# Optimization experiments

Measured on AMD Instinct MI355X. Metric: run time of the kernel, lower is better.

Reference implementation:

```python
import jax, jax.numpy as jnp
import numpy as np
import math

B, S, D = 2, 2048, 1024
H, HD = 16, 64
ROT = 16          # rotary_dim = head_dim * 0.25
FF = 4096
EPS = 1e-5


def setup_inputs() -> dict:
    key = jax.random.key(0)
    ks = jax.random.split(key, 12)
    sc = lambda *sh: 0.02
    inp = {
        "x": jax.random.normal(ks[0], (B, S, D), jnp.float32),
        "attention_mask": jnp.tril(jnp.ones((S, S), bool))[None, None],  # causal [1,1,S,S]
        "W_qkv": jax.random.normal(ks[1], (3 * D, D), jnp.float32) * 0.02,
        "b_qkv": jnp.zeros((3 * D,), jnp.float32),
        "W_o": jax.random.normal(ks[2], (D, D), jnp.float32) * 0.02,
        "b_o": jnp.zeros((D,), jnp.float32),
        "ln1_w": jnp.ones((D,), jnp.float32),
        "ln1_b": jnp.zeros((D,), jnp.float32),
        "ln2_w": jnp.ones((D,), jnp.float32),
        "ln2_b": jnp.zeros((D,), jnp.float32),
        "W1": jax.random.normal(ks[3], (FF, D), jnp.float32) * 0.02,
        "b1": jnp.zeros((FF,), jnp.float32),
        "W2": jax.random.normal(ks[4], (D, FF), jnp.float32) * 0.02,
        "b2": jnp.zeros((D,), jnp.float32),
    }
    # real rotary frequencies, shaped [1,1,S,ROT//2,2]
    inv_freq = 1.0 / (10000.0 ** (jnp.arange(0, ROT, 2, dtype=jnp.float32) / ROT))
    t = jnp.arange(S, dtype=jnp.float32)
    ang = t[:, None] * inv_freq[None, :]                      # [S, ROT//2]
    inp["freqs_cis"] = jnp.stack([jnp.cos(ang), jnp.sin(ang)], -1)[None, None]
    return inp


def layer_norm(x, w, b):
    mu = jnp.mean(x, -1, keepdims=True)
    var = jnp.mean(jnp.square(x - mu), -1, keepdims=True)
    return (x - mu) * jax.lax.rsqrt(var + EPS) * w + b


def apply_rotate_emb(x, freqs_cis):
    # x: [B,H,S,ROT]; freqs_cis: [1,1,S,ROT//2,2]
    x1, x2 = x[..., : ROT // 2], x[..., ROT // 2 :]
    cos, sin = freqs_cis[..., 0], freqs_cis[..., 1]
    return jnp.concatenate([x1 * cos - x2 * sin, x1 * sin + x2 * cos], -1)


def reference(x, attention_mask, freqs_cis, W_qkv, b_qkv, W_o, b_o,
              ln1_w, ln1_b, ln2_w, ln2_b, W1, b1, W2, b2):
    h = layer_norm(x, ln1_w, ln1_b)
    qkv = jnp.einsum("bsd,ed->bse", h, W_qkv) + b_qkv
    q, k, v = jnp.split(qkv, 3, axis=-1)
    to_heads = lambda t: t.reshape(B, S, H, HD).transpose(0, 2, 1, 3)  # [B,H,S,HD]
    q, k, v = to_heads(q), to_heads(k), to_heads(v)
    q = jnp.concatenate([apply_rotate_emb(q[..., :ROT], freqs_cis), q[..., ROT:]], -1)
    k = jnp.concatenate([apply_rotate_emb(k[..., :ROT], freqs_cis), k[..., ROT:]], -1)
    scores = jnp.einsum("bhqd,bhkd->bhqk", q, k) / math.sqrt(HD)
    scores = jnp.where(attention_mask, scores, -jnp.inf)
    probs = jax.nn.softmax(scores, axis=-1)
    out = jnp.einsum("bhqk,bhkd->bhqd", probs, v)
    out = out.transpose(0, 2, 1, 3).reshape(B, S, D)
    attn_out = jnp.einsum("bsd,ed->bse", out, W_o) + b_o
    # parallel residual (dropout is identity in eval)
    h2 = layer_norm(x, ln2_w, ln2_b)
    ff = jnp.einsum("bsf,df->bsd", jax.nn.gelu(jnp.einsum("bsd,fd->bsf", h2, W1) + b1, approximate=False), W2) + b2
    return x + ff + attn_out
```

## Files before the change

kernel.cpp:

```cpp
#include <hip/hip_runtime.h>

#define DEV __device__ __forceinline__

typedef __bf16 bf16;
typedef bf16 bf16x4 __attribute__((ext_vector_type(4)));
typedef bf16 bf16x8 __attribute__((ext_vector_type(8)));
typedef float f32x4 __attribute__((ext_vector_type(4)));

DEV f32x4 mfma16(bf16x8 a, bf16x8 b, f32x4 c) {
  return __builtin_amdgcn_mfma_f32_16x16x32_bf16(a, b, c, 0, 0, 0);
}

DEV void gload_lds16(const bf16* g, bf16* l) {
  __builtin_amdgcn_global_load_lds((const __attribute__((address_space(1))) void*)g,
                                   (__attribute__((address_space(3))) void*)l, 16, 0, 0);
}

#define PH_BAR __builtin_amdgcn_s_barrier()
#define VM(NSTR) asm volatile("s_waitcnt vmcnt(" NSTR ")" ::: "memory")
#define WAITBAR(NSTR) asm volatile("s_waitcnt vmcnt(" NSTR ")\n\ts_barrier" ::: "memory")

DEV float fast_gelu(float x) {
  const float z = x * x;
  const float w = __builtin_fmaf(z, 0.1029353f, 2.3019853f);
  const float e = __builtin_amdgcn_exp2f(x * w);
  const float r = __builtin_amdgcn_rcpf(1.0f + e);
  return x - x * r;
}

__global__ __launch_bounds__(256) void ln_dual(
    const float* __restrict__ x,
    const float* __restrict__ w1, const float* __restrict__ b1,
    const float* __restrict__ w2, const float* __restrict__ b2,
    bf16* __restrict__ h1, bf16* __restrict__ h2)
{
  __shared__ float red[2][4];
  const int row = blockIdx.x, t = threadIdx.x;
  const int lane = t & 63, wave = t >> 6;
  const float4 v = ((const float4*)(x + (size_t)row * 1024))[t];
  float vv[4] = {v.x, v.y, v.z, v.w};
  float s = vv[0] + vv[1] + vv[2] + vv[3];
  float q = vv[0]*vv[0] + vv[1]*vv[1] + vv[2]*vv[2] + vv[3]*vv[3];
  #pragma unroll
  for (int o = 32; o; o >>= 1) { s += __shfl_xor(s, o); q += __shfl_xor(q, o); }
  if (lane == 0) { red[0][wave] = s; red[1][wave] = q; }
  __syncthreads();
  s = red[0][0] + red[0][1] + red[0][2] + red[0][3];
  q = red[1][0] + red[1][1] + red[1][2] + red[1][3];
  const float mu = s * (1.0f / 1024.0f);
  const float var = q * (1.0f / 1024.0f) - mu * mu;
  const float rs = rsqrtf(var + 1e-5f);
  bf16x4 o1, o2;
  #pragma unroll
  for (int j = 0; j < 4; ++j) {
    const int i = t * 4 + j;
    const float xh = (vv[j] - mu) * rs;
    o1[j] = (bf16)(xh * w1[i] + b1[i]);
    o2[j] = (bf16)(xh * w2[i] + b2[i]);
  }
  *(bf16x4*)&h1[(size_t)row * 1024 + t * 4] = o1;
  *(bf16x4*)&h2[(size_t)row * 1024 + t * 4] = o2;
}

__global__ __launch_bounds__(256) void cast_all(
    const float* __restrict__ Wqkv_f, const float* __restrict__ W1_f,
    const float* __restrict__ Wo_f, const float* __restrict__ W2_f,
    bf16* __restrict__ wQKV, bf16* __restrict__ w1, bf16* __restrict__ wCat)
{
  const int b = blockIdx.x, t = threadIdx.x;
  if (b < 3072) {
    const int i = b * 256 + t;
    const float4 v = ((const float4*)Wqkv_f)[i];
    bf16x4 o = {(bf16)v.x, (bf16)v.y, (bf16)v.z, (bf16)v.w};
    ((bf16x4*)wQKV)[i] = o;
  } else if (b < 7168) {
    const int i = (b - 3072) * 256 + t;
    const float4 v = ((const float4*)W1_f)[i];
    bf16x4 o = {(bf16)v.x, (bf16)v.y, (bf16)v.z, (bf16)v.w};
    ((bf16x4*)w1)[i] = o;
  } else if (b < 8192) {
    const int row = b - 7168;
    const float4 v = *(const float4*)&Wo_f[(size_t)row * 1024 + t * 4];
    bf16x4 o = {(bf16)v.x, (bf16)v.y, (bf16)v.z, (bf16)v.w};
    *(bf16x4*)&wCat[(size_t)row * 5120 + t * 4] = o;
  } else {
    const int row = b - 8192;
    #pragma unroll
    for (int k = 0; k < 4; ++k) {
      const int col = t * 4 + k * 1024;
      const float4 v = *(const float4*)&W2_f[(size_t)row * 4096 + col];
      bf16x4 o = {(bf16)v.x, (bf16)v.y, (bf16)v.z, (bf16)v.w};
      *(bf16x4*)&wCat[(size_t)row * 5120 + 1024 + col] = o;
    }
  }
}

DEV bf16x8 ldfrag(const bf16* unit, int lr, int g) {
  return *(const bf16x8*)&unit[lr * 32 + ((g ^ ((lr >> 1) & 3)) << 3)];
}
DEV void read_bfr(const bf16* unit, int blr, int g, bf16x8 bfr[4]) {
  #pragma unroll
  for (int nj = 0; nj < 4; ++nj) bfr[nj] = ldfrag(unit, blr + nj * 16, g);
}
DEV void read_af(const bf16* unit, int alr, int g, bf16x8 af[4]) {
  #pragma unroll
  for (int ml = 0; ml < 4; ++ml) af[ml] = ldfrag(unit, alr + ml * 16, g);
}
DEV void do_mfma(const bf16x8 af[4], const bf16x8 bfr[4], f32x4 acc[8][4], int mh) {
  __builtin_amdgcn_s_setprio(1);
  #pragma unroll
  for (int ml = 0; ml < 4; ++ml)
    #pragma unroll
    for (int nj = 0; nj < 4; ++nj)
      acc[mh * 4 + ml][nj] = mfma16(af[ml], bfr[nj], acc[mh * 4 + ml][nj]);
  __builtin_amdgcn_s_setprio(0);
}

template <int EPI>
__global__ __launch_bounds__(512) void gemm256(
    const bf16* __restrict__ A, const bf16* __restrict__ B,
    const float* __restrict__ bias, void* __restrict__ Cv,
    float* __restrict__ P1, float* __restrict__ P2, float* __restrict__ P3,
    int K, int ldc, int ntiles, int nbx, int nkt)
{
  __shared__ __align__(16) bf16 As[2][2][2][4096];
  __shared__ __align__(16) bf16 Bs[2][2][2][4096];
  const int tid = threadIdx.x;
  const int lane = tid & 63, wave = tid >> 6;
  const int wm = wave >> 2, wn = wave & 3;
  const int g = lane >> 4, c = lane & 15;
  const int cpx = gridDim.x >> 3;
  const int swz = ((int)blockIdx.x & 7) * cpx + ((int)blockIdx.x >> 3);
  const int tile = swz % ntiles;
  const int sk = swz / ntiles;
  const int bm = (tile / nbx) * 256, bn = (tile % nbx) * 256;

  const int slr = tid >> 2;
  const int sch = (tid & 3) ^ ((tid >> 3) & 3);
  const bf16* aU[2][2];
  const bf16* bU[2][2];
  {
    const bf16* a0 = A + (size_t)(bm + ((slr >> 6) * 128) + (slr & 63)) * K
                       + (size_t)sk * nkt * 64 + sch * 8;
    const bf16* b0 = B + (size_t)(bn + slr) * K + (size_t)sk * nkt * 64 + sch * 8;
    aU[0][0] = a0;            aU[0][1] = a0 + (size_t)64 * K;
    aU[1][0] = a0 + 32;       aU[1][1] = a0 + (size_t)64 * K + 32;
    bU[0][0] = b0;            bU[0][1] = b0 + (size_t)128 * K;
    bU[1][0] = b0 + 32;       bU[1][1] = b0 + (size_t)128 * K + 32;
  }
#define STG_A(bf_, kkh_, ub_, ko_) gload_lds16(aU[kkh_][ub_] + (ko_), &As[bf_][kkh_][ub_][wave * 512])
#define STG_B(bf_, kkh_, ub_, ko_) gload_lds16(bU[kkh_][ub_] + (ko_), &Bs[bf_][kkh_][ub_][wave * 512])

  f32x4 acc[8][4] = {};
  bf16x8 bfr[4], af[4];
  const int alr = (wm << 6) + c;
  const int blr = ((wn & 1) << 6) + c;
  const int bub = wn >> 1;

  STG_B(0, 0, 0, 0); STG_B(0, 0, 1, 0); STG_A(0, 0, 0, 0); STG_A(0, 0, 1, 0);
  STG_B(0, 1, 0, 0); STG_B(0, 1, 1, 0); STG_A(0, 1, 0, 0); STG_A(0, 1, 1, 0);
  WAITBAR("4");

  for (int t = 0; t < nkt - 1; ++t) {
    const int buf = t & 1, nxt = buf ^ 1;
    const int ko = (t + 1) * 64;
    read_bfr(&Bs[buf][0][bub][0], blr, g, bfr);
    read_af(&As[buf][0][0][0], alr, g, af);
    STG_B(nxt, 0, 0, ko); STG_B(nxt, 0, 1, ko);
    PH_BAR;
    do_mfma(af, bfr, acc, 0);
    PH_BAR;
    read_af(&As[buf][0][1][0], alr, g, af);
    STG_A(nxt, 0, 0, ko); STG_A(nxt, 0, 1, ko);
    PH_BAR;
    do_mfma(af, bfr, acc, 1);
    VM("4");
    PH_BAR;
    read_bfr(&Bs[buf][1][bub][0], blr, g, bfr);
    read_af(&As[buf][1][0][0], alr, g, af);
    STG_B(nxt, 1, 0, ko); STG_B(nxt, 1, 1, ko);
    PH_BAR;
    do_mfma(af, bfr, acc, 0);
    PH_BAR;
    read_af(&As[buf][1][1][0], alr, g, af);
    STG_A(nxt, 1, 0, ko); STG_A(nxt, 1, 1, ko);
    PH_BAR;
    do_mfma(af, bfr, acc, 1);
    VM("4");
    PH_BAR;
  }
  {
    const int buf = (nkt - 1) & 1;
    read_bfr(&Bs[buf][0][bub][0], blr, g, bfr);
    read_af(&As[buf][0][0][0], alr, g, af);
    PH_BAR;
    do_mfma(af, bfr, acc, 0);
    PH_BAR;
    read_af(&As[buf][0][1][0], alr, g, af);
    PH_BAR;
    do_mfma(af, bfr, acc, 1);
    VM("0");
    PH_BAR;
    read_bfr(&Bs[buf][1][bub][0], blr, g, bfr);
    read_af(&As[buf][1][0][0], alr, g, af);
    PH_BAR;
    do_mfma(af, bfr, acc, 0);
    PH_BAR;
    read_af(&As[buf][1][1][0], alr, g, af);
    PH_BAR;
    do_mfma(af, bfr, acc, 1);
  }
#undef STG_A
#undef STG_B

  float* Pp = nullptr;
  if constexpr (EPI == 2) Pp = (sk == 1) ? P1 : (sk == 2) ? P2 : (sk == 3) ? P3 : (float*)Cv;
  const int row0 = bm + wm * 128 + 4 * g;
  const int col0 = bn + wn * 64 + c;
  #pragma unroll
  for (int mi = 0; mi < 8; ++mi) {
    #pragma unroll
    for (int nj = 0; nj < 4; ++nj) {
      const int col = col0 + nj * 16;
      float bv = 0.0f;
      if constexpr (EPI < 2) bv = bias[col];
      #pragma unroll
      for (int r = 0; r < 4; ++r) {
        const size_t idx = (size_t)(row0 + mi * 16 + r) * ldc + col;
        float vo = acc[mi][nj][r] + bv;
        if constexpr (EPI == 0) {
          ((bf16*)Cv)[idx] = (bf16)vo;
        } else if constexpr (EPI == 1) {
          ((bf16*)Cv)[idx] = (bf16)fast_gelu(vo);
        } else {
          Pp[idx] = vo;
        }
      }
    }
  }
}

__global__ __launch_bounds__(256) void combine_out(
    const float* __restrict__ p0, const float* __restrict__ p1,
    const float* __restrict__ p2, const float* __restrict__ x,
    const float* __restrict__ bo, const float* __restrict__ b2,
    float* __restrict__ out)
{
  const int row = blockIdx.x, t = threadIdx.x;
  const size_t base = (size_t)row * 1024 + t * 4;
  float4 a = *(float4*)&out[base];
  const float4 v0 = *(const float4*)&p0[base];
  const float4 v1 = *(const float4*)&p1[base];
  const float4 v2 = *(const float4*)&p2[base];
  const float4 vx = *(const float4*)&x[base];
  const float4 vb = *(const float4*)&bo[t * 4];
  const float4 vc = *(const float4*)&b2[t * 4];
  a.x += v0.x + v1.x + v2.x + vx.x + vb.x + vc.x;
  a.y += v0.y + v1.y + v2.y + vx.y + vb.y + vc.y;
  a.z += v0.z + v1.z + v2.z + vx.z + vb.z + vc.z;
  a.w += v0.w + v1.w + v2.w + vx.w + vb.w + vc.w;
  *(float4*)&out[base] = a;
}

__global__ __launch_bounds__(256) void rope_reshape(
    const bf16* __restrict__ qkv, const float* __restrict__ freqs,
    bf16* __restrict__ Q, bf16* __restrict__ K, bf16* __restrict__ VT)
{
  __shared__ bf16 vt[64][72];
  const int t = threadIdx.x;
  const int bh = blockIdx.y, b = bh >> 4, h = bh & 15;
  const int sc = blockIdx.x * 64;
  const int sl = t >> 2, s = sc + sl;
  const int d0 = (t & 3) * 16;

  const size_t rowbase = (size_t)(b * 2048 + s) * 3072 + h * 64 + d0;
  const size_t obase = ((size_t)bh * 2048 + s) * 64 + d0;

  #pragma unroll
  for (int which = 0; which < 2; ++which) {
    const bf16* src = qkv + rowbase + which * 1024;
    bf16x8 v0 = *(const bf16x8*)src;
    bf16x8 v1 = *(const bf16x8*)(src + 8);
    if (d0 == 0) {
      bf16x8 r0, r1;
      #pragma unroll
      for (int j = 0; j < 8; ++j) {
        const float cs = freqs[s * 16 + j * 2];
        const float sn = freqs[s * 16 + j * 2 + 1];
        const float x1 = (float)v0[j], x2 = (float)v1[j];
        r0[j] = (bf16)(x1 * cs - x2 * sn);
        r1[j] = (bf16)(x1 * sn + x2 * cs);
      }
      v0 = r0; v1 = r1;
    }
    bf16* dst = (which == 0 ? Q : K) + obase;
    *(bf16x8*)dst = v0;
    *(bf16x8*)(dst + 8) = v1;
  }
  {
    const bf16* src = qkv + rowbase + 2048;
    bf16x8 v0 = *(const bf16x8*)src;
    bf16x8 v1 = *(const bf16x8*)(src + 8);
    #pragma unroll
    for (int j = 0; j < 8; ++j) { vt[sl][d0 + j] = v0[j]; vt[sl][d0 + 8 + j] = v1[j]; }
  }
  __syncthreads();
  {
    const int d = t >> 2;
    const int s0 = (t & 3) * 16;
    bf16x8 o0, o1;
    #pragma unroll
    for (int j = 0; j < 8; ++j) { o0[j] = vt[s0 + j][d]; o1[j] = vt[s0 + 8 + j][d]; }
    bf16* dst = VT + ((size_t)bh * 64 + d) * 2048 + sc + s0;
    *(bf16x8*)dst = o0;
    *(bf16x8*)(dst + 8) = o1;
  }
}

__global__ __launch_bounds__(512, 4) void attn_kernel(
    const bf16* __restrict__ Q, const bf16* __restrict__ Kg,
    const bf16* __restrict__ VTg, bf16* __restrict__ O, int ldO)
{
  __shared__ __align__(16) bf16 Ks[3][64][64];
  __shared__ __align__(16) bf16 Vs[3][64][64];
  __shared__ __align__(16) bf16 Ps[8][16][64];

  const int tid = threadIdx.x;
  const int lane = tid & 63, wave = tid >> 6;
  const int g = lane >> 4, c = lane & 15;
  const int L = blockIdx.x;
  const int half = L >> 8, r = L & 255;
  const int bh = (half << 4) | (r >> 4);
  const int qtile = half ? (15 - (r & 15)) : (r & 15);
  const int qw = qtile * 128 + wave * 16;

  const bf16* Qp = Q + (size_t)bh * 2048 * 64;
  const bf16* Kp = Kg + (size_t)bh * 2048 * 64;
  const bf16* Vp = VTg + (size_t)bh * 64 * 2048;

  const int srow = lane >> 3;
  const int schunk = (lane & 7) ^ srow;
  const int svr = wave * 8 + srow;
  const size_t kdelta = (size_t)64 * 64;

  bf16x8 qreg[2];
  {
    const float qs = 0.125f * 1.44269504f;
    bf16x8 t0 = *(const bf16x8*)&Qp[(size_t)(qw + c) * 64 + g * 8];
    bf16x8 t1 = *(const bf16x8*)&Qp[(size_t)(qw + c) * 64 + 32 + g * 8];
    #pragma unroll
    for (int j = 0; j < 8; ++j) {
      qreg[0][j] = (bf16)((float)t0[j] * qs);
      qreg[1][j] = (bf16)((float)t1[j] * qs);
    }
  }
  bf16x8 ones;
  #pragma unroll
  for (int j = 0; j < 8; ++j) ones[j] = (bf16)1.0f;

  const int cq = c & 7;
  int fo[4][2];
  #pragma unroll
  for (int i = 0; i < 4; ++i)
    #pragma unroll
    for (int kk = 0; kk < 2; ++kk)
      fo[i][kk] = (i * 16 + c) * 64 + (((kk * 4 + g) ^ cq) << 3);
  bf16* pw[4];
  #pragma unroll
  for (int kf = 0; kf < 4; ++kf)
    pw[kf] = &Ps[wave][c][((((kf * 2 + (g >> 1)) ^ cq) << 3)) + ((g & 1) << 2)];
  const bf16* pr[2];
  #pragma unroll
  for (int kk = 0; kk < 2; ++kk)
    pr[kk] = &Ps[wave][c][((kk * 4 + g) ^ cq) << 3];
  const bf16* ks0 = &Ks[0][0][0];
  const bf16* vs0 = &Vs[0][0][0];

  f32x4 oacc[4] = {};
  f32x4 lacc = {};
  float m_ = -1e30f;

  const int nkb = 2 * qtile + 2;
#define STAGE(j_, b3_) do {                                                        \
    gload_lds16(&Kp[(size_t)((j_) * 64 + svr) * 64 + schunk * 8], &Ks[b3_][wave * 8][0]); \
    gload_lds16(&Vp[(size_t)svr * 2048 + (j_) * 64 + schunk * 8], &Vs[b3_][wave * 8][0]); \
  } while (0)

  auto qkt = [&](f32x4* st, int bufi) {
    const bf16* kt = ks0 + bufi * kdelta;
    __builtin_amdgcn_s_setprio(1);
    #pragma unroll
    for (int kf = 0; kf < 4; ++kf) {
      f32x4 z = {};
      z = mfma16(*(const bf16x8*)(kt + fo[kf][0]), qreg[0], z);
      st[kf] = mfma16(*(const bf16x8*)(kt + fo[kf][1]), qreg[1], z);
    }
    __builtin_amdgcn_s_setprio(0);
  };

  auto smpv = [&](const f32x4* st, int j_, int bufi) {
    const int kbase = j_ * 64;
    float v[16];
    if (kbase + 63 > qw) {
      const int qrel = qw + c - kbase;
      #pragma unroll
      for (int kf = 0; kf < 4; ++kf)
        #pragma unroll
        for (int rr = 0; rr < 4; ++rr)
          v[kf * 4 + rr] = (kf * 16 + 4 * g + rr <= qrel) ? st[kf][rr] : -1e30f;
    } else {
      #pragma unroll
      for (int kf = 0; kf < 4; ++kf)
        #pragma unroll
        for (int rr = 0; rr < 4; ++rr)
          v[kf * 4 + rr] = st[kf][rr];
    }
    float u0 = fmaxf(fmaxf(v[0], v[1]), v[2]);
    float u1 = fmaxf(fmaxf(v[3], v[4]), v[5]);
    float u2 = fmaxf(fmaxf(v[6], v[7]), v[8]);
    float u3 = fmaxf(fmaxf(v[9], v[10]), v[11]);
    float u4 = fmaxf(fmaxf(v[12], v[13]), v[14]);
    float tm = fmaxf(fmaxf(fmaxf(u0, u1), u2), fmaxf(fmaxf(u3, u4), v[15]));
    if (__any(tm > m_ + 8.0f)) {
      float tr = fmaxf(tm, __shfl_xor(tm, 16));
      tr = fmaxf(tr, __shfl_xor(tr, 32));
      const float mn = fmaxf(m_, tr);
      const float alpha = __builtin_amdgcn_exp2f(m_ - mn);
      m_ = mn;
      lacc[0] *= alpha; lacc[1] *= alpha; lacc[2] *= alpha; lacc[3] *= alpha;
      #pragma unroll
      for (int df = 0; df < 4; ++df) {
        oacc[df][0] *= alpha; oacc[df][1] *= alpha;
        oacc[df][2] *= alpha; oacc[df][3] *= alpha;
      }
    }
    bf16 p[16];
    #pragma unroll
    for (int i = 0; i < 16; ++i)
      p[i] = (bf16)__builtin_amdgcn_exp2f(v[i] - m_);
    #pragma unroll
    for (int kf = 0; kf < 4; ++kf) {
      bf16x4 pk = {p[kf * 4], p[kf * 4 + 1], p[kf * 4 + 2], p[kf * 4 + 3]};
      *(bf16x4*)pw[kf] = pk;
    }
    bf16x8 pfrag0 = *(const bf16x8*)pr[0];
    bf16x8 pfrag1 = *(const bf16x8*)pr[1];
    const bf16* vt = vs0 + bufi * kdelta;
    __builtin_amdgcn_s_setprio(1);
    #pragma unroll
    for (int df = 0; df < 4; ++df) {
      oacc[df] = mfma16(*(const bf16x8*)(vt + fo[df][0]), pfrag0, oacc[df]);
      oacc[df] = mfma16(*(const bf16x8*)(vt + fo[df][1]), pfrag1, oacc[df]);
    }
    lacc = mfma16(ones, pfrag0, lacc);
    lacc = mfma16(ones, pfrag1, lacc);
    __builtin_amdgcn_s_setprio(0);
  };

  f32x4 stA[4], stB[4];
  STAGE(0, 0);
  STAGE(1, 1);
  VM("0");
  PH_BAR;
  qkt(stA, 0);

  const int nit = nkb >> 1;
  for (int i = 0; i < nit; ++i) {
    const int jA = 2 * i, jB = 2 * i + 1;
    if (jA + 2 < nkb) STAGE(jA + 2, (jA + 2) % 3);
    if (jB * 64 <= qw + 15) qkt(stB, jB % 3);
    if (jA * 64 <= qw + 15) smpv(stA, jA, jA % 3);
    VM("0");
    PH_BAR;
    if (jB + 2 < nkb) STAGE(jB + 2, (jB + 2) % 3);
    if (jB + 1 < nkb && (jB + 1) * 64 <= qw + 15) qkt(stA, (jB + 1) % 3);
    if (jB * 64 <= qw + 15) smpv(stB, jB, jB % 3);
    VM("0");
    PH_BAR;
  }
#undef STAGE

  const int b = bh >> 4, h = bh & 15;
  const float inv = 1.0f / lacc[0];
  const int s = qw + c;
  #pragma unroll
  for (int df = 0; df < 4; ++df) {
    bf16x4 o;
    #pragma unroll
    for (int rr = 0; rr < 4; ++rr) o[rr] = (bf16)(oacc[df][rr] * inv);
    *(bf16x4*)&O[(size_t)(b * 2048 + s) * ldO + h * 64 + df * 16 + 4 * g] = o;
  }
}

extern "C" void kernel_launch(void* const* d_in, const int* in_sizes, int n_in,
                              void* d_out, int out_size, void* d_ws, size_t ws_size,
                              hipStream_t stream) {
  const float* x     = (const float*)d_in[0];
  const float* W_qkv = (const float*)d_in[2];
  const float* b_qkv = (const float*)d_in[3];
  const float* W_o   = (const float*)d_in[4];
  const float* b_o   = (const float*)d_in[5];
  const float* ln1w  = (const float*)d_in[6];
  const float* ln1b  = (const float*)d_in[7];
  const float* ln2w  = (const float*)d_in[8];
  const float* ln2b  = (const float*)d_in[9];
  const float* W1    = (const float*)d_in[10];
  const float* b1    = (const float*)d_in[11];
  const float* W2    = (const float*)d_in[12];
  const float* b2    = (const float*)d_in[13];
  const float* freqs = (const float*)d_in[14];
  float* out = (float*)d_out;

  char* ws = (char*)d_ws;
  const size_t MB = (size_t)1 << 20;
  bf16* h1   = (bf16*)(ws + 0 * MB);
  bf16* h2   = (bf16*)(ws + 8 * MB);
  bf16* wQKV = (bf16*)(ws + 16 * MB);
  bf16* wCat = (bf16*)(ws + 22 * MB);
  bf16* w1   = (bf16*)(ws + 32 * MB);
  bf16* qkv  = (bf16*)(ws + 40 * MB);
  bf16* Qb   = (bf16*)(ws + 64 * MB);
  bf16* Kb   = (bf16*)(ws + 72 * MB);
  bf16* VTb  = (bf16*)(ws + 80 * MB);
  bf16* A2   = (bf16*)(ws + 88 * MB);
  float* p0  = (float*)(ws + 0 * MB);
  float* p1  = (float*)(ws + 40 * MB);
  float* p2  = (float*)(ws + 64 * MB);

  ln_dual<<<4096, 256, 0, stream>>>(x, ln1w, ln1b, ln2w, ln2b, h1, h2);
  cast_all<<<9216, 256, 0, stream>>>(W_qkv, W1, W_o, W2, wQKV, w1, wCat);

  gemm256<0><<<192, 512, 0, stream>>>(h1, wQKV, b_qkv, qkv,
                                      nullptr, nullptr, nullptr,
                                      1024, 3072, 192, 12, 16);
  rope_reshape<<<dim3(32, 32), 256, 0, stream>>>(qkv, freqs, Qb, Kb, VTb);
  attn_kernel<<<512, 512, 0, stream>>>(Qb, Kb, VTb, A2, 5120);
  gemm256<1><<<256, 512, 0, stream>>>(h2, w1, b1, A2 + 1024,
                                      nullptr, nullptr, nullptr,
                                      1024, 5120, 256, 16, 16);
  gemm256<2><<<256, 512, 0, stream>>>(A2, wCat, nullptr, p0,
                                      p1, p2, out,
                                      5120, 1024, 64, 4, 20);
  combine_out<<<4096, 256, 0, stream>>>(p0, p1, p2, x, b_o, b2, out);
}
```

Baseline: 206.0 us.

## Fuse LN with weight cast, store split-K partials in bf16, deepen attention pipeline

Merges the layernorm and weight-cast kernels into one launch. The split-K output GEMM now writes bf16 partials to four buffers, where before it wrote fp32 partials and accumulated into the output, which roughly halves partial-sum traffic in the combine step. Attention K/V staging goes from triple to quadruple buffering so loads are issued one stage earlier with a partial vmcnt wait. The risks are precision loss from rounding the partial sums to bf16 and extra LDS use in attention, which may lower occupancy.

```diff
diff --git a/kernel.cpp b/kernel.cpp
--- a/kernel.cpp
+++ b/kernel.cpp
@@ -28,63 +28,62 @@
   return x - x * r;
 }
 
-__global__ __launch_bounds__(256) void ln_dual(
+__global__ __launch_bounds__(256) void ln_cast_all(
     const float* __restrict__ x,
-    const float* __restrict__ w1, const float* __restrict__ b1,
-    const float* __restrict__ w2, const float* __restrict__ b2,
-    bf16* __restrict__ h1, bf16* __restrict__ h2)
-{
-  __shared__ float red[2][4];
-  const int row = blockIdx.x, t = threadIdx.x;
-  const int lane = t & 63, wave = t >> 6;
-  const float4 v = ((const float4*)(x + (size_t)row * 1024))[t];
-  float vv[4] = {v.x, v.y, v.z, v.w};
-  float s = vv[0] + vv[1] + vv[2] + vv[3];
-  float q = vv[0]*vv[0] + vv[1]*vv[1] + vv[2]*vv[2] + vv[3]*vv[3];
-  #pragma unroll
-  for (int o = 32; o; o >>= 1) { s += __shfl_xor(s, o); q += __shfl_xor(q, o); }
-  if (lane == 0) { red[0][wave] = s; red[1][wave] = q; }
-  __syncthreads();
-  s = red[0][0] + red[0][1] + red[0][2] + red[0][3];
-  q = red[1][0] + red[1][1] + red[1][2] + red[1][3];
-  const float mu = s * (1.0f / 1024.0f);
-  const float var = q * (1.0f / 1024.0f) - mu * mu;
-  const float rs = rsqrtf(var + 1e-5f);
-  bf16x4 o1, o2;
-  #pragma unroll
-  for (int j = 0; j < 4; ++j) {
-    const int i = t * 4 + j;
-    const float xh = (vv[j] - mu) * rs;
-    o1[j] = (bf16)(xh * w1[i] + b1[i]);
-    o2[j] = (bf16)(xh * w2[i] + b2[i]);
-  }
-  *(bf16x4*)&h1[(size_t)row * 1024 + t * 4] = o1;
-  *(bf16x4*)&h2[(size_t)row * 1024 + t * 4] = o2;
-}
-
-__global__ __launch_bounds__(256) void cast_all(
+    const float* __restrict__ ln1w, const float* __restrict__ ln1b,
+    const float* __restrict__ ln2w, const float* __restrict__ ln2b,
+    bf16* __restrict__ h1, bf16* __restrict__ h2,
     const float* __restrict__ Wqkv_f, const float* __restrict__ W1_f,
     const float* __restrict__ Wo_f, const float* __restrict__ W2_f,
     bf16* __restrict__ wQKV, bf16* __restrict__ w1, bf16* __restrict__ wCat)
 {
   const int b = blockIdx.x, t = threadIdx.x;
-  if (b < 3072) {
-    const int i = b * 256 + t;
+  if (b < 4096) {
+    __shared__ float red[2][4];
+    const int lane = t & 63, wave = t >> 6;
+    const float4 v = ((const float4*)(x + (size_t)b * 1024))[t];
+    float vv[4] = {v.x, v.y, v.z, v.w};
+    float s = vv[0] + vv[1] + vv[2] + vv[3];
+    float q = vv[0]*vv[0] + vv[1]*vv[1] + vv[2]*vv[2] + vv[3]*vv[3];
+    #pragma unroll
+    for (int o = 32; o; o >>= 1) { s += __shfl_xor(s, o); q += __shfl_xor(q, o); }
+    if (lane == 0) { red[0][wave] = s; red[1][wave] = q; }
+    __syncthreads();
+    s = red[0][0] + red[0][1] + red[0][2] + red[0][3];
+    q = red[1][0] + red[1][1] + red[1][2] + red[1][3];
+    const float mu = s * (1.0f / 1024.0f);
+    const float var = q * (1.0f / 1024.0f) - mu * mu;
+    const float rs = rsqrtf(var + 1e-5f);
+    bf16x4 o1, o2;
+    #pragma unroll
+    for (int j = 0; j < 4; ++j) {
+      const int i = t * 4 + j;
+      const float xh = (vv[j] - mu) * rs;
+      o1[j] = (bf16)(xh * ln1w[i] + ln1b[i]);
+      o2[j] = (bf16)(xh * ln2w[i] + ln2b[i]);
+    }
+    *(bf16x4*)&h1[(size_t)b * 1024 + t * 4] = o1;
+    *(bf16x4*)&h2[(size_t)b * 1024 + t * 4] = o2;
+    return;
+  }
+  const int cb = b - 4096;
+  if (cb < 3072) {
+    const int i = cb * 256 + t;
     const float4 v = ((const float4*)Wqkv_f)[i];
     bf16x4 o = {(bf16)v.x, (bf16)v.y, (bf16)v.z, (bf16)v.w};
     ((bf16x4*)wQKV)[i] = o;
-  } else if (b < 7168) {
-    const int i = (b - 3072) * 256 + t;
+  } else if (cb < 7168) {
+    const int i = (cb - 3072) * 256 + t;
     const float4 v = ((const float4*)W1_f)[i];
     bf16x4 o = {(bf16)v.x, (bf16)v.y, (bf16)v.z, (bf16)v.w};
     ((bf16x4*)w1)[i] = o;
-  } else if (b < 8192) {
-    const int row = b - 7168;
+  } else if (cb < 8192) {
+    const int row = cb - 7168;
     const float4 v = *(const float4*)&Wo_f[(size_t)row * 1024 + t * 4];
     bf16x4 o = {(bf16)v.x, (bf16)v.y, (bf16)v.z, (bf16)v.w};
     *(bf16x4*)&wCat[(size_t)row * 5120 + t * 4] = o;
   } else {
-    const int row = b - 8192;
+    const int row = cb - 8192;
     #pragma unroll
     for (int k = 0; k < 4; ++k) {
       const int col = t * 4 + k * 1024;
@@ -120,7 +119,7 @@
 __global__ __launch_bounds__(512) void gemm256(
     const bf16* __restrict__ A, const bf16* __restrict__ B,
     const float* __restrict__ bias, void* __restrict__ Cv,
-    float* __restrict__ P1, float* __restrict__ P2, float* __restrict__ P3,
+    void* __restrict__ P1, void* __restrict__ P2, void* __restrict__ P3,
     int K, int ldc, int ntiles, int nbx, int nkt)
 {
   __shared__ __align__(16) bf16 As[2][2][2][4096];
@@ -213,8 +212,9 @@
 #undef STG_A
 #undef STG_B
 
-  float* Pp = nullptr;
-  if constexpr (EPI == 2) Pp = (sk == 1) ? P1 : (sk == 2) ? P2 : (sk == 3) ? P3 : (float*)Cv;
+  bf16* Pp = nullptr;
+  if constexpr (EPI == 2)
+    Pp = (bf16*)((sk == 1) ? P1 : (sk == 2) ? P2 : (sk == 3) ? P3 : Cv);
   const int row0 = bm + wm * 128 + 4 * g;
   const int col0 = bn + wn * 64 + c;
   #pragma unroll
@@ -233,7 +233,7 @@
         } else if constexpr (EPI == 1) {
           ((bf16*)Cv)[idx] = (bf16)fast_gelu(vo);
         } else {
-          Pp[idx] = vo;
+          Pp[idx] = (bf16)vo;
         }
       }
     }
@@ -241,25 +241,27 @@
 }
 
 __global__ __launch_bounds__(256) void combine_out(
-    const float* __restrict__ p0, const float* __restrict__ p1,
-    const float* __restrict__ p2, const float* __restrict__ x,
+    const bf16* __restrict__ q0, const bf16* __restrict__ q1,
+    const bf16* __restrict__ q2, const bf16* __restrict__ q3,
+    const float* __restrict__ x,
     const float* __restrict__ bo, const float* __restrict__ b2,
     float* __restrict__ out)
 {
   const int row = blockIdx.x, t = threadIdx.x;
   const size_t base = (size_t)row * 1024 + t * 4;
-  float4 a = *(float4*)&out[base];
-  const float4 v0 = *(const float4*)&p0[base];
-  const float4 v1 = *(const float4*)&p1[base];
-  const float4 v2 = *(const float4*)&p2[base];
+  const bf16x4 a0 = *(const bf16x4*)&q0[base];
+  const bf16x4 a1 = *(const bf16x4*)&q1[base];
+  const bf16x4 a2 = *(const bf16x4*)&q2[base];
+  const bf16x4 a3 = *(const bf16x4*)&q3[base];
   const float4 vx = *(const float4*)&x[base];
   const float4 vb = *(const float4*)&bo[t * 4];
   const float4 vc = *(const float4*)&b2[t * 4];
-  a.x += v0.x + v1.x + v2.x + vx.x + vb.x + vc.x;
-  a.y += v0.y + v1.y + v2.y + vx.y + vb.y + vc.y;
-  a.z += v0.z + v1.z + v2.z + vx.z + vb.z + vc.z;
-  a.w += v0.w + v1.w + v2.w + vx.w + vb.w + vc.w;
-  *(float4*)&out[base] = a;
+  float4 o;
+  o.x = (float)a0[0] + (float)a1[0] + (float)a2[0] + (float)a3[0] + vx.x + vb.x + vc.x;
+  o.y = (float)a0[1] + (float)a1[1] + (float)a2[1] + (float)a3[1] + vx.y + vb.y + vc.y;
+  o.z = (float)a0[2] + (float)a1[2] + (float)a2[2] + (float)a3[2] + vx.z + vb.z + vc.z;
+  o.w = (float)a0[3] + (float)a1[3] + (float)a2[3] + (float)a3[3] + vx.w + vb.w + vc.w;
+  *(float4*)&out[base] = o;
 }
 
 __global__ __launch_bounds__(256) void rope_reshape(
@@ -321,8 +323,8 @@
     const bf16* __restrict__ Q, const bf16* __restrict__ Kg,
     const bf16* __restrict__ VTg, bf16* __restrict__ O, int ldO)
 {
-  __shared__ __align__(16) bf16 Ks[3][64][64];
-  __shared__ __align__(16) bf16 Vs[3][64][64];
+  __shared__ __align__(16) bf16 Ks[4][64][64];
+  __shared__ __align__(16) bf16 Vs[4][64][64];
   __shared__ __align__(16) bf16 Ps[8][16][64];
 
   const int tid = threadIdx.x;
@@ -381,9 +383,9 @@
   float m_ = -1e30f;
 
   const int nkb = 2 * qtile + 2;
-#define STAGE(j_, b3_) do {                                                        \
-    gload_lds16(&Kp[(size_t)((j_) * 64 + svr) * 64 + schunk * 8], &Ks[b3_][wave * 8][0]); \
-    gload_lds16(&Vp[(size_t)svr * 2048 + (j_) * 64 + schunk * 8], &Vs[b3_][wave * 8][0]); \
+#define STAGE(j_) do { const int b4_ = (j_) & 3;                                   \
+    gload_lds16(&Kp[(size_t)((j_) * 64 + svr) * 64 + schunk * 8], &Ks[b4_][wave * 8][0]); \
+    gload_lds16(&Vp[(size_t)svr * 2048 + (j_) * 64 + schunk * 8], &Vs[b4_][wave * 8][0]); \
   } while (0)
 
   auto qkt = [&](f32x4* st, int bufi) {
@@ -458,24 +460,25 @@
   };
 
   f32x4 stA[4], stB[4];
-  STAGE(0, 0);
-  STAGE(1, 1);
-  VM("0");
+  STAGE(0); STAGE(1); STAGE(2);
+  VM("2");
   PH_BAR;
   qkt(stA, 0);
 
   const int nit = nkb >> 1;
   for (int i = 0; i < nit; ++i) {
     const int jA = 2 * i, jB = 2 * i + 1;
-    if (jA + 2 < nkb) STAGE(jA + 2, (jA + 2) % 3);
-    if (jB * 64 <= qw + 15) qkt(stB, jB % 3);
-    if (jA * 64 <= qw + 15) smpv(stA, jA, jA % 3);
-    VM("0");
-    PH_BAR;
-    if (jB + 2 < nkb) STAGE(jB + 2, (jB + 2) % 3);
-    if (jB + 1 < nkb && (jB + 1) * 64 <= qw + 15) qkt(stA, (jB + 1) % 3);
-    if (jB * 64 <= qw + 15) smpv(stB, jB, jB % 3);
-    VM("0");
+    const bool stgA = (jA + 3 < nkb);
+    if (stgA) STAGE(jA + 3);
+    if (jB * 64 <= qw + 15) qkt(stB, jB & 3);
+    smpv(stA, jA, jA & 3);
+    if (stgA) { VM("2"); } else { VM("0"); }
+    PH_BAR;
+    const bool stgB = (jB + 3 < nkb);
+    if (stgB) STAGE(jB + 3);
+    if (jB + 1 < nkb && (jB + 1) * 64 <= qw + 15) qkt(stA, (jB + 1) & 3);
+    if (jB * 64 <= qw + 15) smpv(stB, jB, jB & 3);
+    if (stgB) { VM("2"); } else { VM("0"); }
     PH_BAR;
   }
 #undef STAGE
@@ -523,12 +526,13 @@
   bf16* Kb   = (bf16*)(ws + 72 * MB);
   bf16* VTb  = (bf16*)(ws + 80 * MB);
   bf16* A2   = (bf16*)(ws + 88 * MB);
-  float* p0  = (float*)(ws + 0 * MB);
-  float* p1  = (float*)(ws + 40 * MB);
-  float* p2  = (float*)(ws + 64 * MB);
-
-  ln_dual<<<4096, 256, 0, stream>>>(x, ln1w, ln1b, ln2w, ln2b, h1, h2);
-  cast_all<<<9216, 256, 0, stream>>>(W_qkv, W1, W_o, W2, wQKV, w1, wCat);
+  bf16* q0   = (bf16*)(ws + 0 * MB);
+  bf16* q1   = (bf16*)(ws + 8 * MB);
+  bf16* q2   = (bf16*)(ws + 40 * MB);
+  bf16* q3   = (bf16*)(ws + 48 * MB);
+
+  ln_cast_all<<<13312, 256, 0, stream>>>(x, ln1w, ln1b, ln2w, ln2b, h1, h2,
+                                         W_qkv, W1, W_o, W2, wQKV, w1, wCat);
 
   gemm256<0><<<192, 512, 0, stream>>>(h1, wQKV, b_qkv, qkv,
                                       nullptr, nullptr, nullptr,
@@ -538,8 +542,8 @@
   gemm256<1><<<256, 512, 0, stream>>>(h2, w1, b1, A2 + 1024,
                                       nullptr, nullptr, nullptr,
                                       1024, 5120, 256, 16, 16);
-  gemm256<2><<<256, 512, 0, stream>>>(A2, wCat, nullptr, p0,
-                                      p1, p2, out,
+  gemm256<2><<<256, 512, 0, stream>>>(A2, wCat, nullptr, q0,
+                                      q1, q2, q3,
                                       5120, 1024, 64, 4, 20);
-  combine_out<<<4096, 256, 0, stream>>>(p0, p1, p2, x, b_o, b2, out);
-}
+  combine_out<<<4096, 256, 0, stream>>>(q0, q1, q2, q3, x, b_o, b2, out);
+}
```

Result: faster. 196.4 us (-4.6%).
